# Kernel optimization log

Hardware: AMD Instinct MI355X
Metric: run time of the kernel (lower is better)

The kernel has to match this reference:

```python
import jax, jax.numpy as jnp
import numpy as np

EPS = 1e-6

def setup_inputs() -> dict:
    key = jax.random.key(0)
    ks = jax.random.split(key, 9)
    B, T, D = 4, 1024, 128
    sc = 1.0 / np.sqrt(D)
    return {
        "x_seq": jax.random.normal(ks[0], (B, T, D), dtype=jnp.float32),
        "Wq": jax.random.uniform(ks[1], (D, D), jnp.float32, -sc, sc),
        "bq": jax.random.uniform(ks[2], (D,), jnp.float32, -sc, sc),
        "Wk": jax.random.uniform(ks[3], (D, D), jnp.float32, -sc, sc),
        "bk": jax.random.uniform(ks[4], (D,), jnp.float32, -sc, sc),
        "Wv": jax.random.uniform(ks[5], (D, D), jnp.float32, -sc, sc),
        "bv": jax.random.uniform(ks[6], (D,), jnp.float32, -sc, sc),
        "Wa": jax.random.uniform(ks[7], (D, D), jnp.float32, -sc, sc),
        "ba": jax.random.uniform(ks[8], (D,), jnp.float32, -sc, sc),
    }

def reference(x_seq, Wq, bq, Wk, bk, Wv, bv, Wa, ba):
    B, T, D = x_seq.shape
    q = jax.nn.relu(x_seq @ Wq.T + bq)          # [B,T,D]
    k = jax.nn.relu(x_seq @ Wk.T + bk)
    v = x_seq @ Wv.T + bv
    A = jax.nn.sigmoid(x_seq @ Wa.T + ba)       # per-step decay gate

    def step(carry, inp):
        s, z = carry                             # s:[B,D,D], z:[B,D]
        a_t, k_t, v_t, q_t = inp                 # each [B,D]
        s = a_t[:, :, None] * s + k_t[:, :, None] * v_t[:, None, :]  # s[b,i,j]=a_i*s + k_i v_j
        z = a_t * z + k_t
        num = jnp.einsum('bi,bij->bj', q_t, s)
        den = jnp.sum(q_t * z, axis=-1, keepdims=True) + EPS
        return (s, z), num / den

    s0 = jnp.zeros((B, D, D), x_seq.dtype)
    z0 = jnp.zeros((B, D), x_seq.dtype)
    xs = (jnp.swapaxes(A, 0, 1), jnp.swapaxes(k, 0, 1),
          jnp.swapaxes(v, 0, 1), jnp.swapaxes(q, 0, 1))  # time-major [T,B,D]
    _, y = jax.lax.scan(step, (s0, z0), xs)
    return jnp.swapaxes(y, 0, 1)                 # [B,T,D]
```

## Files before the change

### kernel.cpp

```cpp
#include <hip/hip_runtime.h>

#define BB 4
#define TT 1024
#define DD 128
#define LL 16
#define CC 64
#define EPSV 1e-6f

#define BTD (BB*TT*DD)
#define BCD (BB*CC*DD)

#define OFF_QC   0
#define OFF_KH   (OFF_QC + BTD)
#define OFF_V    (OFF_KH + BTD)
#define OFF_G    (OFF_V  + BTD)
#define OFF_CL   (OFF_G  + BTD)
#define OFF_KS   (OFF_CL + BCD)
#define OFF_Z0   (OFF_KS + BCD)
#define OFF_KBT  (OFF_Z0 + BCD)
#define OFF_S0   (OFF_KBT + BTD)

__global__ __launch_bounds__(256) void k_gemm(
    const float* __restrict__ x,
    const float* __restrict__ Wq, const float* __restrict__ bq,
    const float* __restrict__ Wk, const float* __restrict__ bk,
    const float* __restrict__ Wv, const float* __restrict__ bv,
    const float* __restrict__ Wa, const float* __restrict__ ba,
    float* __restrict__ ws)
{
    __shared__ float xs [32][DD];
    __shared__ float wsh[64][132];

    const int tid = threadIdx.x;
    const int bx  = blockIdx.x;
    const int rt  = bx >> 3;
    const int mt  = bx & 7;
    const int m   = mt >> 1;
    const int jh  = mt & 1;

    const float* W    = (m==0)?Wq : (m==1)?Wk : (m==2)?Wv : Wa;
    const float* bias = (m==0)?bq : (m==1)?bk : (m==2)?bv : ba;

    {
        const float4* xg = (const float4*)(x + (size_t)rt*32*DD);
        #pragma unroll
        for (int r=0;r<4;r++){
            int f = tid + r*256;
            *(float4*)&xs[f>>5][(f&31)*4] = xg[f];
        }
        const float4* wg = (const float4*)(W + (size_t)jh*64*DD);
        #pragma unroll
        for (int r=0;r<8;r++){
            int f = tid + r*256;
            *(float4*)&wsh[f>>5][(f&31)*4] = wg[f];
        }
    }
    __syncthreads();

    const int ci = tid & 15;
    const int ri = tid >> 4;

    float acc[2][4];
    #pragma unroll
    for (int cc=0;cc<4;cc++){
        float bv_ = bias[jh*64 + ci + 16*cc];
        acc[0][cc]=bv_; acc[1][cc]=bv_;
    }

    #pragma unroll 2
    for (int k4=0; k4<32; k4++){
        float4 xa = *(const float4*)&xs[ri   ][k4*4];
        float4 xb = *(const float4*)&xs[ri+16][k4*4];
        #pragma unroll
        for (int cc=0;cc<4;cc++){
            float4 w = *(const float4*)&wsh[ci+16*cc][k4*4];
            acc[0][cc] = fmaf(xa.x,w.x, fmaf(xa.y,w.y, fmaf(xa.z,w.z, fmaf(xa.w,w.w, acc[0][cc]))));
            acc[1][cc] = fmaf(xb.x,w.x, fmaf(xb.y,w.y, fmaf(xb.z,w.z, fmaf(xb.w,w.w, acc[1][cc]))));
        }
    }

    float* dst = ws + ((m==0)?OFF_QC : (m==1)?OFF_KH : (m==2)?OFF_V : OFF_G);
    #pragma unroll
    for (int rr=0;rr<2;rr++){
        int row = rt*32 + ri + 16*rr;
        #pragma unroll
        for (int cc=0;cc<4;cc++){
            float v = acc[rr][cc];
            if (m==0 || m==1) v = fmaxf(v, 0.f);
            else if (m==3)    v = 1.f/(1.f+__expf(-v));
            dst[(size_t)row*DD + jh*64 + ci + 16*cc] = v;
        }
    }
}

__global__ __launch_bounds__(256) void k_chunk(float* __restrict__ ws)
{
    __shared__ float qs [LL][64];
    __shared__ float krs[LL][64];
    __shared__ float gs [LL][64];
    __shared__ float kbs[LL][64];

    const int tid = threadIdx.x;
    const int bh  = blockIdx.x;
    const int bc  = bh >> 1;
    const int jh  = bh & 1;
    const int jbase = jh*64;
    const int b   = bc / CC;
    const int t0  = (bc % CC) * LL;
    const size_t tile = (size_t)(b*TT + t0)*DD;

    {
        const int t = tid >> 4, c4 = (tid & 15)*4;
        const size_t off = tile + (size_t)t*DD + jbase + c4;
        *(float4*)&qs [t][c4] = *(const float4*)(ws + OFF_QC + off);
        *(float4*)&krs[t][c4] = *(const float4*)(ws + OFF_KH + off);
        *(float4*)&gs [t][c4] = *(const float4*)(ws + OFF_G  + off);
    }
    __syncthreads();

    if (tid < 64){
        float c = 1.f;
        #pragma unroll
        for (int t=0;t<LL;t++){ c *= gs[t][tid]; gs[t][tid] = c; }
        ws[OFF_CL + (size_t)bc*DD + jbase + tid] = c;
    }
    __syncthreads();

    {
        const int col = tid & 63;
        const int tg  = tid >> 6;
        const float cl = gs[LL-1][col];
        #pragma unroll
        for (int r=0;r<4;r++){
            int t = tg*4 + r;
            float cv = gs[t][col];
            ws[OFF_QC + tile + (size_t)t*DD + jbase + col] = qs[t][col] * cv;
            float kh = krs[t][col] / cv;
            ws[OFF_KH + tile + (size_t)t*DD + jbase + col] = kh;
            kbs[t][col] = kh * cl;
        }
    }
    __syncthreads();

    if (tid < 64){
        float s = 0.f;
        #pragma unroll
        for (int t=0;t<LL;t++) s += kbs[t][tid];
        ws[OFF_KS + (size_t)bc*DD + jbase + tid] = s;
    }
    {
        const int il = tid >> 2;
        const int tg = tid & 3;
        float4 v;
        v.x = kbs[tg*4+0][il];
        v.y = kbs[tg*4+1][il];
        v.z = kbs[tg*4+2][il];
        v.w = kbs[tg*4+3][il];
        *(float4*)(ws + OFF_KBT + ((size_t)(b*DD + jbase + il)*TT + t0 + tg*4)) = v;
    }
}

__global__ __launch_bounds__(128) void k_scan(float* __restrict__ ws)
{
    __shared__ float kbt[TT];
    __shared__ float cls[CC], kss[CC];

    const int bi = blockIdx.x;
    const int b  = bi >> 7;
    const int i  = bi & 127;
    const int j  = threadIdx.x;

    {
        const float4* src = (const float4*)(ws + OFF_KBT + (size_t)(b*DD + i)*TT);
        ((float4*)kbt)[j]     = src[j];
        ((float4*)kbt)[j+128] = src[j+128];
        if (j < CC) cls[j]    = ws[OFF_CL + (size_t)(b*CC + j)*DD + i];
        else        kss[j-CC] = ws[OFF_KS + (size_t)(b*CC + j-CC)*DD + i];
    }
    __syncthreads();

    const float* Vg = ws + OFF_V + (size_t)b*TT*DD + j;
    float* s0 = ws + OFF_S0 + (size_t)b*CC*DD*DD + (size_t)i*DD + j;
    float* z0 = ws + OFF_Z0;

    float s = 0.f, z = 0.f;
    float vA[16], vB[16];

#define LOADV(dst, ch) { \
        _Pragma("unroll") \
        for (int u=0;u<16;u++) dst[u] = Vg[(size_t)((ch)*LL+u)*DD]; }

#define STEP(vv, ch) { \
        float p0 = kbt[(ch)*16+ 0]*vv[ 0] + kbt[(ch)*16+ 4]*vv[ 4] \
                 + kbt[(ch)*16+ 8]*vv[ 8] + kbt[(ch)*16+12]*vv[12]; \
        float p1 = kbt[(ch)*16+ 1]*vv[ 1] + kbt[(ch)*16+ 5]*vv[ 5] \
                 + kbt[(ch)*16+ 9]*vv[ 9] + kbt[(ch)*16+13]*vv[13]; \
        float p2 = kbt[(ch)*16+ 2]*vv[ 2] + kbt[(ch)*16+ 6]*vv[ 6] \
                 + kbt[(ch)*16+10]*vv[10] + kbt[(ch)*16+14]*vv[14]; \
        float p3 = kbt[(ch)*16+ 3]*vv[ 3] + kbt[(ch)*16+ 7]*vv[ 7] \
                 + kbt[(ch)*16+11]*vv[11] + kbt[(ch)*16+15]*vv[15]; \
        float Ue = (p0+p1)+(p2+p3); \
        s0[(size_t)(ch)*DD*DD] = s; \
        if (j==0) z0[(size_t)(b*CC+(ch))*DD + i] = z; \
        s = fmaf(cls[ch], s, Ue); \
        z = fmaf(cls[ch], z, kss[ch]); }

    LOADV(vA, 0);
    for (int ch=0; ch<CC; ch+=2){
        LOADV(vB, ch+1);
        STEP(vA, ch);
        if (ch+2 < CC) LOADV(vA, ch+2);
        STEP(vB, ch+1);
    }
#undef LOADV
#undef STEP
}

__global__ __launch_bounds__(256) void k_out(const float* __restrict__ ws, float* __restrict__ y)
{
    __shared__ float qcs[LL][DD+4];
    __shared__ float khs[LL][DD+4];
    __shared__ float vsm[LL][64+4];
    __shared__ float Ss[LL][LL];
    __shared__ float denS[LL];
    __shared__ float z0s[DD];
    __shared__ float s0s[2][32][64+4];

    const int tid = threadIdx.x;
    const int bh  = blockIdx.x;
    const int bc  = bh >> 1;
    const int jh  = bh & 1;
    const int jbase = jh * 64;
    const int b   = bc / CC;
    const int ch  = bc % CC;
    const int t0  = ch * LL;
    const size_t tile = (size_t)(b*TT + t0)*DD;
    const float* s0g = ws + OFF_S0 + (size_t)bc*DD*DD;

    float4 pre[2];
    {
        const float4* qcg = (const float4*)(ws + OFF_QC + tile);
        const float4* khg = (const float4*)(ws + OFF_KH + tile);
        #pragma unroll
        for (int rep=0; rep<2; rep++){
            int f = tid + rep*256;
            int t = f >> 5, k4 = f & 31;
            *(float4*)&qcs[t][k4*4] = qcg[f];
            *(float4*)&khs[t][k4*4] = khg[f];
        }
        {
            int t = tid >> 4, c = (tid & 15)*4;
            *(float4*)&vsm[t][c] =
                *(const float4*)(ws + OFF_V + tile + (size_t)t*DD + jbase + c);
        }
        if (tid < DD) z0s[tid] = ws[OFF_Z0 + (size_t)bc*DD + tid];
        #pragma unroll
        for (int r=0;r<2;r++){
            int f = tid + r*256;
            int row = f >> 4, c4 = (f & 15)*4;
            pre[r] = *(const float4*)(s0g + (size_t)row*DD + jbase + c4);
        }
    }
    __syncthreads();

    {
        int t = tid >> 4, u = tid & 15;
        float s = 0.f;
        #pragma unroll 8
        for (int k4=0; k4<32; k4++){
            float4 q4 = *(const float4*)&qcs[t][k4*4];
            float4 h4 = *(const float4*)&khs[u][k4*4];
            s = fmaf(q4.x,h4.x, fmaf(q4.y,h4.y, fmaf(q4.z,h4.z, fmaf(q4.w,h4.w, s))));
        }
        Ss[t][u] = (u <= t) ? s : 0.f;
    }
    __syncthreads();

    if (tid < LL){
        int t = tid;
        float d = EPSV;
        for (int u=0; u<=t; u++) d += Ss[t][u];
        #pragma unroll 8
        for (int kk=0; kk<DD; kk++) d += qcs[t][kk]*z0s[kk];
        denS[t] = d;
    }

    const int t  = tid >> 4;
    const int jg = tid & 15;
    const int j0 = jg * 4;
    float y4[4] = {0.f,0.f,0.f,0.f};

    __syncthreads();
    #pragma unroll
    for (int u=0; u<LL; u++){
        float sv = Ss[t][u];
        float4 v4 = *(const float4*)&vsm[u][j0];
        y4[0]=fmaf(sv,v4.x,y4[0]); y4[1]=fmaf(sv,v4.y,y4[1]);
        y4[2]=fmaf(sv,v4.z,y4[2]); y4[3]=fmaf(sv,v4.w,y4[3]);
    }

    #pragma unroll
    for (int sl=0; sl<4; sl++){
        __syncthreads();
        #pragma unroll
        for (int r=0;r<2;r++){
            int f = tid + r*256;
            *(float4*)&s0s[sl&1][f>>4][(f&15)*4] = pre[r];
        }
        if (sl < 3){
            #pragma unroll
            for (int r=0;r<2;r++){
                int f = tid + r*256;
                int row = f >> 4, c4 = (f & 15)*4;
                pre[r] = *(const float4*)(s0g + (size_t)((sl+1)*32 + row)*DD + jbase + c4);
            }
        }
        __syncthreads();
        #pragma unroll 8
        for (int ii=0; ii<32; ii++){
            float qv = qcs[t][sl*32+ii];
            float4 s4 = *(const float4*)&s0s[sl&1][ii][j0];
            y4[0]=fmaf(qv,s4.x,y4[0]); y4[1]=fmaf(qv,s4.y,y4[1]);
            y4[2]=fmaf(qv,s4.z,y4[2]); y4[3]=fmaf(qv,s4.w,y4[3]);
        }
    }

    const float rd = 1.f/denS[t];
    float* yg = y + tile + (size_t)t*DD + jbase + j0;
    *(float4*)yg = make_float4(y4[0]*rd, y4[1]*rd, y4[2]*rd, y4[3]*rd);
}

extern "C" void kernel_launch(void* const* d_in, const int* in_sizes, int n_in,
                              void* d_out, int out_size, void* d_ws, size_t ws_size,
                              hipStream_t stream)
{
    const float* x  = (const float*)d_in[0];
    const float* Wq = (const float*)d_in[1]; const float* bq = (const float*)d_in[2];
    const float* Wk = (const float*)d_in[3]; const float* bk = (const float*)d_in[4];
    const float* Wv = (const float*)d_in[5]; const float* bv = (const float*)d_in[6];
    const float* Wa = (const float*)d_in[7]; const float* ba = (const float*)d_in[8];
    float* ws = (float*)d_ws;
    float* yo = (float*)d_out;

    hipLaunchKernelGGL(k_gemm,  dim3(1024),    dim3(256), 0, stream,
                       x, Wq,bq, Wk,bk, Wv,bv, Wa,ba, ws);
    hipLaunchKernelGGL(k_chunk, dim3(BB*CC*2), dim3(256), 0, stream, ws);
    hipLaunchKernelGGL(k_scan,  dim3(BB*DD),   dim3(128), 0, stream, ws);
    hipLaunchKernelGGL(k_out,   dim3(BB*CC*2), dim3(256), 0, stream, ws, yo);
}
```

Before: 128.7 us.

## Precompute per-chunk KV outer products in chunk kernel, simplify state scan

The per-chunk update U = sum_t kb_t ⊗ v_t moves from the sequential scan kernel into the parallel chunk kernel, which now loads V into shared memory and writes a full B×C×D×D U tensor to global memory. The scan kernel then only streams U with a 16-deep register prefetch and does one FMA per chunk, instead of recomputing 16-term dot products from V and a transposed kb buffer. This trades extra global traffic (a 16 MB U write plus read) for removing redundant V reloads across 128 scan blocks and shortening the serial dependency chain.

Measured after the change: 115.2 us. 10.5% less time.

```diff
diff --git a/kernel.cpp b/kernel.cpp
--- a/kernel.cpp
+++ b/kernel.cpp
@@ -17,8 +17,8 @@
 #define OFF_CL   (OFF_G  + BTD)
 #define OFF_KS   (OFF_CL + BCD)
 #define OFF_Z0   (OFF_KS + BCD)
-#define OFF_KBT  (OFF_Z0 + BCD)
-#define OFF_S0   (OFF_KBT + BTD)
+#define OFF_U    (OFF_Z0 + BCD)
+#define OFF_S0   (OFF_U  + BB*CC*DD*DD)
 
 __global__ __launch_bounds__(256) void k_gemm(
     const float* __restrict__ x,
@@ -98,23 +98,27 @@
     __shared__ float qs [LL][64];
     __shared__ float krs[LL][64];
     __shared__ float gs [LL][64];
+    __shared__ float vs [LL][DD];
     __shared__ float kbs[LL][64];
 
     const int tid = threadIdx.x;
     const int bh  = blockIdx.x;
     const int bc  = bh >> 1;
-    const int jh  = bh & 1;
-    const int jbase = jh*64;
+    const int h   = bh & 1;
+    const int ibase = h*64;
     const int b   = bc / CC;
     const int t0  = (bc % CC) * LL;
     const size_t tile = (size_t)(b*TT + t0)*DD;
 
     {
         const int t = tid >> 4, c4 = (tid & 15)*4;
-        const size_t off = tile + (size_t)t*DD + jbase + c4;
+        const size_t off = tile + (size_t)t*DD + ibase + c4;
         *(float4*)&qs [t][c4] = *(const float4*)(ws + OFF_QC + off);
         *(float4*)&krs[t][c4] = *(const float4*)(ws + OFF_KH + off);
         *(float4*)&gs [t][c4] = *(const float4*)(ws + OFF_G  + off);
+        const int tv = tid >> 5, cv = (tid & 31)*4;
+        *(float4*)&vs[tv  ][cv] = *(const float4*)(ws + OFF_V + tile + (size_t)tv*DD + cv);
+        *(float4*)&vs[tv+8][cv] = *(const float4*)(ws + OFF_V + tile + (size_t)(tv+8)*DD + cv);
     }
     __syncthreads();
 
@@ -122,7 +126,7 @@
         float c = 1.f;
         #pragma unroll
         for (int t=0;t<LL;t++){ c *= gs[t][tid]; gs[t][tid] = c; }
-        ws[OFF_CL + (size_t)bc*DD + jbase + tid] = c;
+        ws[OFF_CL + (size_t)bc*DD + ibase + tid] = c;
     }
     __syncthreads();
 
@@ -134,9 +138,9 @@
         for (int r=0;r<4;r++){
             int t = tg*4 + r;
             float cv = gs[t][col];
-            ws[OFF_QC + tile + (size_t)t*DD + jbase + col] = qs[t][col] * cv;
+            ws[OFF_QC + tile + (size_t)t*DD + ibase + col] = qs[t][col] * cv;
             float kh = krs[t][col] / cv;
-            ws[OFF_KH + tile + (size_t)t*DD + jbase + col] = kh;
+            ws[OFF_KH + tile + (size_t)t*DD + ibase + col] = kh;
             kbs[t][col] = kh * cl;
         }
     }
@@ -146,74 +150,63 @@
         float s = 0.f;
         #pragma unroll
         for (int t=0;t<LL;t++) s += kbs[t][tid];
-        ws[OFF_KS + (size_t)bc*DD + jbase + tid] = s;
-    }
-    {
-        const int il = tid >> 2;
-        const int tg = tid & 3;
-        float4 v;
-        v.x = kbs[tg*4+0][il];
-        v.y = kbs[tg*4+1][il];
-        v.z = kbs[tg*4+2][il];
-        v.w = kbs[tg*4+3][il];
-        *(float4*)(ws + OFF_KBT + ((size_t)(b*DD + jbase + il)*TT + t0 + tg*4)) = v;
+        ws[OFF_KS + (size_t)bc*DD + ibase + tid] = s;
+    }
+
+    const int j  = tid & 127;
+    const int ih = tid >> 7;
+    float vr[LL];
+    #pragma unroll
+    for (int u=0;u<LL;u++) vr[u]=vs[u][j];
+    float* Ug = ws + OFF_U + (size_t)bc*DD*DD;
+    #pragma unroll
+    for (int i4=0;i4<8;i4++){
+        int il = ih*32 + i4*4;
+        float a0=0.f,a1=0.f,a2=0.f,a3=0.f;
+        #pragma unroll
+        for (int u=0;u<LL;u++){
+            float4 kb4 = *(const float4*)(&kbs[u][il]);
+            float vu = vr[u];
+            a0 = fmaf(kb4.x,vu,a0); a1 = fmaf(kb4.y,vu,a1);
+            a2 = fmaf(kb4.z,vu,a2); a3 = fmaf(kb4.w,vu,a3);
+        }
+        Ug[(size_t)(ibase+il+0)*DD + j]=a0; Ug[(size_t)(ibase+il+1)*DD + j]=a1;
+        Ug[(size_t)(ibase+il+2)*DD + j]=a2; Ug[(size_t)(ibase+il+3)*DD + j]=a3;
     }
 }
 
 __global__ __launch_bounds__(128) void k_scan(float* __restrict__ ws)
 {
-    __shared__ float kbt[TT];
     __shared__ float cls[CC], kss[CC];
-
     const int bi = blockIdx.x;
     const int b  = bi >> 7;
     const int i  = bi & 127;
     const int j  = threadIdx.x;
 
-    {
-        const float4* src = (const float4*)(ws + OFF_KBT + (size_t)(b*DD + i)*TT);
-        ((float4*)kbt)[j]     = src[j];
-        ((float4*)kbt)[j+128] = src[j+128];
-        if (j < CC) cls[j]    = ws[OFF_CL + (size_t)(b*CC + j)*DD + i];
-        else        kss[j-CC] = ws[OFF_KS + (size_t)(b*CC + j-CC)*DD + i];
-    }
-    __syncthreads();
-
-    const float* Vg = ws + OFF_V + (size_t)b*TT*DD + j;
-    float* s0 = ws + OFF_S0 + (size_t)b*CC*DD*DD + (size_t)i*DD + j;
-    float* z0 = ws + OFF_Z0;
+    if (j < CC) cls[j]      = ws[OFF_CL + (size_t)(b*CC + j)*DD + i];
+    else        kss[j - CC] = ws[OFF_KS + (size_t)(b*CC + j - CC)*DD + i];
+    __syncthreads();
+
+    const float* U  = ws + OFF_U;
+    float*       s0 = ws + OFF_S0;
+    float*       z0 = ws + OFF_Z0;
+    const size_t base = (size_t)b*CC*DD*DD + (size_t)i*DD + j;
+
+    float up[16];
+    #pragma unroll
+    for (int p=0;p<16;p++) up[p] = U[base + (size_t)p*DD*DD];
 
     float s = 0.f, z = 0.f;
-    float vA[16], vB[16];
-
-#define LOADV(dst, ch) { \
-        _Pragma("unroll") \
-        for (int u=0;u<16;u++) dst[u] = Vg[(size_t)((ch)*LL+u)*DD]; }
-
-#define STEP(vv, ch) { \
-        float p0 = kbt[(ch)*16+ 0]*vv[ 0] + kbt[(ch)*16+ 4]*vv[ 4] \
-                 + kbt[(ch)*16+ 8]*vv[ 8] + kbt[(ch)*16+12]*vv[12]; \
-        float p1 = kbt[(ch)*16+ 1]*vv[ 1] + kbt[(ch)*16+ 5]*vv[ 5] \
-                 + kbt[(ch)*16+ 9]*vv[ 9] + kbt[(ch)*16+13]*vv[13]; \
-        float p2 = kbt[(ch)*16+ 2]*vv[ 2] + kbt[(ch)*16+ 6]*vv[ 6] \
-                 + kbt[(ch)*16+10]*vv[10] + kbt[(ch)*16+14]*vv[14]; \
-        float p3 = kbt[(ch)*16+ 3]*vv[ 3] + kbt[(ch)*16+ 7]*vv[ 7] \
-                 + kbt[(ch)*16+11]*vv[11] + kbt[(ch)*16+15]*vv[15]; \
-        float Ue = (p0+p1)+(p2+p3); \
-        s0[(size_t)(ch)*DD*DD] = s; \
-        if (j==0) z0[(size_t)(b*CC+(ch))*DD + i] = z; \
-        s = fmaf(cls[ch], s, Ue); \
-        z = fmaf(cls[ch], z, kss[ch]); }
-
-    LOADV(vA, 0);
-    for (int ch=0; ch<CC; ch+=2){
-        LOADV(vB, ch+1);
-        STEP(vA, ch);
-        if (ch+2 < CC) LOADV(vA, ch+2);
-        STEP(vB, ch+1);
-    }
-#undef LOADV
-#undef STEP
+    #pragma unroll
+    for (int ch=0; ch<CC; ch++){
+        s0[base + (size_t)ch*DD*DD] = s;
+        if (j==0) z0[(size_t)(b*CC+ch)*DD + i] = z;
+        float u  = up[ch & 15];
+        if (ch + 16 < CC) up[ch & 15] = U[base + (size_t)(ch+16)*DD*DD];
+        float cl = cls[ch];
+        s = fmaf(cl, s, u);
+        z = fmaf(cl, z, kss[ch]);
+    }
 }
 
 __global__ __launch_bounds__(256) void k_out(const float* __restrict__ ws, float* __restrict__ y)
```
